# Performance work log

Measured on AMD Instinct MI355X. Metric: run time of the kernel, lower is better.

The kernel has to match this reference:

```python
import jax, jax.numpy as jnp
import numpy as np

B, N, E, L, H, FA = 64, 29, 812, 9, 256, 5  # batch, max atoms, edges, layers, hidden, atom types
SCALE = 15.0


def _scatter_add(vals, idx):
    # vals [B,E,D], idx [B,E] -> [B,N,D]  (replaces one-hot multiply + reduce_sum)
    return jax.vmap(lambda v, i: jnp.zeros((N, v.shape[-1]), v.dtype).at[i].add(v))(vals, idx)


def _align(x, mask):
    n = jnp.sum(mask, axis=1, keepdims=True)
    mean = jnp.sum(x, axis=1, keepdims=True) / n
    return (x - mean) * mask


def setup_inputs() -> dict:
    key = jax.random.key(0)
    ks = iter(jax.random.split(key, 32))
    # fully connected edges i != j, same graph per batch element
    pairs = np.array([(i, j) for i in range(N) for j in range(N) if i != j], dtype=np.int32)
    edge_indices = jnp.tile(jnp.asarray(pairs)[None], (B, 1, 1))
    x_in = jax.random.normal(next(ks), (B, N, 3), jnp.float32)
    h_in = jax.random.normal(next(ks), (B, N, FA), jnp.float32)
    t = jax.random.uniform(next(ks), (B, N, 1), jnp.float32)
    node_mask = jnp.ones((B, N, 1), jnp.float32)
    edge_mask = jnp.ones((B, E, 1), jnp.float32)

    def w(k, shape, fan):
        return jax.random.normal(k, shape, jnp.float32) / np.float32(np.sqrt(fan))

    params = dict(
        win_w=w(next(ks), (FA + 1, H), FA + 1), win_b=jnp.zeros((H,), jnp.float32),
        wout_w=w(next(ks), (H, FA + 1), H), wout_b=jnp.zeros((FA + 1,), jnp.float32),
        e_w1=w(next(ks), (L, 2 * H + 2, H), 2 * H + 2), e_b1=jnp.zeros((L, H), jnp.float32),
        e_w2=w(next(ks), (L, H, H), H), e_b2=jnp.zeros((L, H), jnp.float32),
        att_w=w(next(ks), (L, H, 1), H), att_b=jnp.zeros((L, 1), jnp.float32),
        h_w1=w(next(ks), (L, 2 * H, H), 2 * H), h_b1=jnp.zeros((L, H), jnp.float32),
        h_w2=w(next(ks), (L, H, H), H), h_b2=jnp.zeros((L, H), jnp.float32),
        x_w1=w(next(ks), (L, 2 * H + 2, H), 2 * H + 2), x_b1=jnp.zeros((L, H), jnp.float32),
        x_w2=w(next(ks), (L, H, H), H), x_b2=jnp.zeros((L, H), jnp.float32),
        x_w3=w(next(ks), (L, H, 1), H),
    )
    return {"x_in": x_in, "h_in": h_in, "t": t, "node_mask": node_mask,
            "edge_mask": edge_mask, "edge_indices": edge_indices, **params}


def _forward(x_in, h_in, t, node_mask, edge_mask, edge_indices, p):
    bidx = jnp.arange(x_in.shape[0])[:, None]
    idx_i, idx_j = edge_indices[..., 0], edge_indices[..., 1]
    h = jnp.concatenate([h_in, t], axis=-1) @ p["win_w"] + p["win_b"]
    x = x_in
    # global pairwise distances, masked (the `a` feature)
    xi0, xj0 = x[bidx, idx_i], x[bidx, idx_j]
    a = jnp.sqrt(jnp.sum((xi0 - xj0) ** 2, axis=-1, keepdims=True)) * edge_mask
    for l in range(L):
        x_i, x_j = x[bidx, idx_i], x[bidx, idx_j]
        diff = (x_i - x_j) * edge_mask              # [B,E,3]
        d = jnp.sqrt(jnp.sum(diff ** 2, axis=-1, keepdims=True))
        h_i, h_j = h[bidx, idx_i], h[bidx, idx_j]
        feat = jnp.concatenate([h_i, h_j, d ** 2, a], axis=-1)  # [B,E,514]
        # --- update_x ---
        u = jax.nn.silu(feat @ p["x_w1"][l] + p["x_b1"][l])
        u = jax.nn.silu(u @ p["x_w2"][l] + p["x_b2"][l])
        u = jnp.tanh(u @ p["x_w3"][l]) * SCALE      # [B,E,1]
        u = u * diff / (d + 1.0)                    # [B,E,3]
        x = (x + _scatter_add(u, idx_i)) * node_mask
        # --- update_h ---
        m = jax.nn.silu(feat @ p["e_w1"][l] + p["e_b1"][l])
        m = jax.nn.silu(m @ p["e_w2"][l] + p["e_b2"][l])
        e = jax.nn.sigmoid(m @ p["att_w"][l] + p["att_b"][l])
        agg = _scatter_add(e * m, idx_i)            # [B,N,256]
        hm = jax.nn.silu(jnp.concatenate([h, agg], axis=-1) @ p["h_w1"][l] + p["h_b1"][l])
        hm = hm @ p["h_w2"][l] + p["h_b2"][l]
        h = (h + hm) * node_mask
    x_out = _align((x - x_in) * node_mask, node_mask)
    h_out = (h @ p["wout_w"] + p["wout_b"]) * node_mask
    return jnp.concatenate([x_out, h_out[..., :-1]], axis=-1)


def reference(x_in, h_in, t, node_mask, edge_mask, edge_indices,
              win_w, win_b, wout_w, wout_b,
              e_w1, e_b1, e_w2, e_b2, att_w, att_b,
              h_w1, h_b1, h_w2, h_b2,
              x_w1, x_b1, x_w2, x_b2, x_w3):
    p = dict(win_w=win_w, win_b=win_b, wout_w=wout_w, wout_b=wout_b,
             e_w1=e_w1, e_b1=e_b1, e_w2=e_w2, e_b2=e_b2,
             att_w=att_w, att_b=att_b,
             h_w1=h_w1, h_b1=h_b1, h_w2=h_w2, h_b2=h_b2,
             x_w1=x_w1, x_b1=x_b1, x_w2=x_w2, x_b2=x_b2, x_w3=x_w3)
    return _forward(x_in, h_in, t, node_mask, edge_mask, edge_indices, p)
```

## Files before the change

kernel.cpp:

```cpp
#include <hip/hip_runtime.h>
#include <math.h>

#define B_ 64
#define N_ 29
#define E_ 812
#define L_ 9
#define H_ 256
#define FA_ 5
#define BN_ (B_*N_)
#define BE_ (B_*E_)
#define DEG_ 28
#define NBAND_ (BN_/64)
#define SCALE_ 15.0f

typedef __attribute__((ext_vector_type(8))) short bf16x8;
typedef __attribute__((ext_vector_type(4))) float f32x4;

__device__ __forceinline__ float sigmoidf_(float v){ return 1.0f/(1.0f+expf(-v)); }
__device__ __forceinline__ float siluf_(float v){ return v/(1.0f+expf(-v)); }
__device__ __forceinline__ float fsilu_(float v){
    float e = __expf(-v);
    return v * __builtin_amdgcn_rcpf(1.0f + e);
}

__device__ __forceinline__ ushort f2bf(float f){
    uint u = __float_as_uint(f);
    u += 0x7fffu + ((u>>16)&1u);
    return (ushort)(u>>16);
}
__device__ __forceinline__ float bf2f(ushort h){ return __uint_as_float(((uint)h)<<16); }

__global__ void k_init_h(const float* __restrict__ h_in, const float* __restrict__ t,
                         const float* __restrict__ win_w, const float* __restrict__ win_b,
                         float* __restrict__ h)
{
    int node = blockIdx.x; int c = threadIdx.x;
    float in[6];
    #pragma unroll
    for (int k=0;k<FA_;k++) in[k] = h_in[node*FA_+k];
    in[5] = t[node];
    float acc = win_b[c];
    #pragma unroll
    for (int k=0;k<6;k++) acc += in[k]*win_w[k*H_+c];
    h[(size_t)node*H_+c] = acc;
}

__global__ void k_init_xa(const float* __restrict__ x_in, const int* __restrict__ eidx,
                          const float* __restrict__ emask, float* __restrict__ x, float* __restrict__ a)
{
    int gid = blockIdx.x*256 + threadIdx.x;
    if (gid < BN_*3) x[gid] = x_in[gid];
    if (gid < BE_) {
        int b = gid / E_;
        int ii = eidx[2*gid], jj = eidx[2*gid+1];
        const float* xi = x_in + (size_t)(b*N_+ii)*3;
        const float* xj = x_in + (size_t)(b*N_+jj)*3;
        float dx = xi[0]-xj[0], dy = xi[1]-xj[1], dz = xi[2]-xj[2];
        a[gid] = sqrtf(dx*dx+dy*dy+dz*dz) * emask[gid];
    }
}

__global__ void k_wprep(const float* __restrict__ xw2, const float* __restrict__ ew2,
                        ushort* __restrict__ WfU, ushort* __restrict__ WfM)
{
    int gid = blockIdx.x*256 + threadIdx.x;
    if (gid >= L_*2*8192) return;
    int lane = gid & 63;
    int rest = gid >> 6;
    int ct = rest & 15; rest >>= 4;
    int ks = rest & 7;  rest >>= 3;
    int p  = rest & 1;  int l = rest >> 1;
    const float* src = (p ? ew2 : xw2) + (size_t)l*H_*H_;
    ushort* dst = (p ? WfM : WfU) + (size_t)l*131072;
    int g = lane>>4, li = lane&15;
    int col = ct*16 + li;
    int kb  = ks*32 + g*8;
    size_t fo = ((size_t)(ks*16+ct)*64 + lane)*8;
    ushort* dh = dst + fo;
    ushort* dl = dst + 65536 + fo;
    #pragma unroll
    for (int j=0;j<8;j++){
        float v = src[(size_t)(kb+j)*H_ + col];
        ushort h = f2bf(v);
        dh[j] = h;
        dl[j] = f2bf(v - bf2f(h));
    }
}

__global__ void k_wprep6(const float* __restrict__ xw1, const float* __restrict__ ew1,
                         const float* __restrict__ hw1, ushort* __restrict__ Wf6)
{
    int gid = blockIdx.x*256 + threadIdx.x;
    if (gid >= L_*5*8192) return;
    int lane = gid & 63;
    int rest = gid >> 6;
    int ct = rest & 15; rest >>= 4;
    int ks = rest & 7;  rest >>= 3;
    int m  = rest % 5;  int l = rest / 5;
    const float* src;
    switch (m) {
        case 0: src = xw1 + (size_t)l*514*H_; break;
        case 1: src = xw1 + (size_t)l*514*H_ + (size_t)256*H_; break;
        case 2: src = ew1 + (size_t)l*514*H_; break;
        case 3: src = ew1 + (size_t)l*514*H_ + (size_t)256*H_; break;
        default: src = hw1 + (size_t)l*512*H_; break;
    }
    ushort* dst = Wf6 + (size_t)(l*5+m)*196608;
    int g = lane>>4, li = lane&15;
    int col = ct*16 + li;
    int kb  = ks*32 + g*8;
    size_t fo = ((size_t)(ks*16+ct)*64 + lane)*8;
    #pragma unroll
    for (int j=0;j<8;j++){
        float v = src[(size_t)(kb+j)*H_ + col];
        ushort h0 = f2bf(v); float r1 = v - bf2f(h0);
        ushort h1 = f2bf(r1); float r2 = r1 - bf2f(h1);
        dst[fo+j] = h0;
        dst[65536+fo+j] = h1;
        dst[131072+fo+j] = f2bf(r2);
    }
}

__global__ void k_hfrag(const float* __restrict__ h,
                        ushort* __restrict__ p0, ushort* __restrict__ p1, ushort* __restrict__ p2)
{
    int gid = blockIdx.x*256 + threadIdx.x;
    if (gid >= BN_*32) return;
    int row = gid >> 5, octet = gid & 31;
    const float* src = h + (size_t)row*H_ + octet*8;
    int band=row>>6, r=row&63, rt=r>>4, li=r&15;
    int ks=octet>>2, gg=octet&3;
    size_t fo = (((size_t)((band*8+ks)*4+rt)*64)+(gg*16+li))*8;
    ushort q0[8], q1[8], q2[8];
    #pragma unroll
    for (int j=0;j<8;j++){
        float v = src[j];
        ushort h0 = f2bf(v); float r1 = v - bf2f(h0);
        ushort h1 = f2bf(r1); float r2 = r1 - bf2f(h1);
        q0[j]=h0; q1[j]=h1; q2[j]=f2bf(r2);
    }
    *(ushort4*)(p0+fo)   = make_ushort4(q0[0],q0[1],q0[2],q0[3]);
    *(ushort4*)(p0+fo+4) = make_ushort4(q0[4],q0[5],q0[6],q0[7]);
    *(ushort4*)(p1+fo)   = make_ushort4(q1[0],q1[1],q1[2],q1[3]);
    *(ushort4*)(p1+fo+4) = make_ushort4(q1[4],q1[5],q1[6],q1[7]);
    *(ushort4*)(p2+fo)   = make_ushort4(q2[0],q2[1],q2[2],q2[3]);
    *(ushort4*)(p2+fo+4) = make_ushort4(q2[4],q2[5],q2[6],q2[7]);
}

struct GArg { const float* A; const float* Bw; const float* bias; const float* add; const float* rmask; float* C; };
struct GArgs { GArg g[6]; };

template<int ACT>
__global__ __launch_bounds__(256)
void k_gemm64(GArgs args, int M, int Kdim)
{
    const GArg ga = args.g[blockIdx.z];
    __shared__ float As[16*68];
    __shared__ float Bs[16*68];
    const int tid = threadIdx.x;
    const int row0 = blockIdx.x*64;
    const int col0 = blockIdx.y*64;
    const int ty = tid>>4, tx = tid&15;
    const int am = tid>>2, ak = (tid&3)<<2;
    const int bk = tid>>4, bn = (tid&15)<<2;
    float acc[4][4] = {};
    const float* Ap = ga.A + (size_t)min(row0+am, M-1)*Kdim + ak;
    const float* Bp = ga.Bw + (size_t)bk*H_ + col0 + bn;
    for (int k0=0; k0<Kdim; k0+=16) {
        float4 av = *(const float4*)(Ap + k0);
        float4 bv = *(const float4*)(Bp + (size_t)k0*H_);
        __syncthreads();
        As[(ak+0)*68+am]=av.x; As[(ak+1)*68+am]=av.y; As[(ak+2)*68+am]=av.z; As[(ak+3)*68+am]=av.w;
        *(float4*)&Bs[bk*68+bn] = bv;
        __syncthreads();
        #pragma unroll
        for (int k=0;k<16;k++) {
            float4 a4 = *(const float4*)&As[k*68 + (ty<<2)];
            float4 b4 = *(const float4*)&Bs[k*68 + (tx<<2)];
            float aa[4]={a4.x,a4.y,a4.z,a4.w};
            float bb[4]={b4.x,b4.y,b4.z,b4.w};
            #pragma unroll
            for (int i=0;i<4;i++)
                #pragma unroll
                for (int j=0;j<4;j++)
                    acc[i][j] = fmaf(aa[i], bb[j], acc[i][j]);
        }
    }
    const int r0 = row0 + (ty<<2);
    const int c0 = col0 + (tx<<2);
    float4 bias4 = make_float4(0.f,0.f,0.f,0.f);
    if (ga.bias) bias4 = *(const float4*)(ga.bias + c0);
    #pragma unroll
    for (int i=0;i<4;i++) {
        int r = r0+i;
        if (r >= M) break;
        float v0=acc[i][0]+bias4.x, v1=acc[i][1]+bias4.y, v2=acc[i][2]+bias4.z, v3=acc[i][3]+bias4.w;
        if (ga.add) {
            float4 ad = *(const float4*)(ga.add + (size_t)r*H_ + c0);
            v0+=ad.x; v1+=ad.y; v2+=ad.z; v3+=ad.w;
        }
        if (ACT==1) { v0=siluf_(v0); v1=siluf_(v1); v2=siluf_(v2); v3=siluf_(v3); }
        if (ga.rmask) { float mv = ga.rmask[r]; v0*=mv; v1*=mv; v2*=mv; v3*=mv; }
        *(float4*)(ga.C + (size_t)r*H_ + c0) = make_float4(v0,v1,v2,v3);
    }
}

struct NArg6 { const ushort* A0; const ushort* A1; const ushort* A2;
               const ushort* Wf; float* Cf; };
struct NArgs6 { NArg6 g[5]; };

__global__ __launch_bounds__(256, 4)
void k_ngemm6(NArgs6 args)
{
    const NArg6 ga = args.g[blockIdx.z];
    const int tid  = threadIdx.x;
    const int lane = tid & 63;
    const int wv   = tid >> 6;
    const int g    = lane >> 4;
    const int li   = lane & 15;
    const int band = blockIdx.x;
    const int row0 = band*64;
    const int ctg  = blockIdx.y*4 + wv;

    const size_t abase = (size_t)band*16384 + (size_t)lane*8;
    const ushort* bp = ga.Wf + (size_t)ctg*512 + (size_t)lane*8;

    f32x4 acc[4];
    #pragma unroll
    for (int rt=0;rt<4;++rt) acc[rt] = (f32x4){0.f,0.f,0.f,0.f};

    #pragma unroll
    for (int ks=0; ks<8; ++ks){
        bf16x8 a0[4], a1[4], a2[4];
        #pragma unroll
        for (int rt=0; rt<4; ++rt){
            size_t o = abase + (size_t)(ks*4+rt)*512;
            a0[rt] = *(const bf16x8*)(ga.A0 + o);
            a1[rt] = *(const bf16x8*)(ga.A1 + o);
            a2[rt] = *(const bf16x8*)(ga.A2 + o);
        }
        bf16x8 b0 = *(const bf16x8*)(bp + ks*8192);
        bf16x8 b1 = *(const bf16x8*)(bp + 65536 + ks*8192);
        bf16x8 b2 = *(const bf16x8*)(bp + 131072 + ks*8192);
        #pragma unroll
        for (int rt=0; rt<4; ++rt){
            acc[rt] = __builtin_amdgcn_mfma_f32_16x16x32_bf16(a0[rt], b0, acc[rt], 0,0,0);
            acc[rt] = __builtin_amdgcn_mfma_f32_16x16x32_bf16(a1[rt], b0, acc[rt], 0,0,0);
            acc[rt] = __builtin_amdgcn_mfma_f32_16x16x32_bf16(a0[rt], b1, acc[rt], 0,0,0);
            acc[rt] = __builtin_amdgcn_mfma_f32_16x16x32_bf16(a1[rt], b1, acc[rt], 0,0,0);
            acc[rt] = __builtin_amdgcn_mfma_f32_16x16x32_bf16(a2[rt], b0, acc[rt], 0,0,0);
            acc[rt] = __builtin_amdgcn_mfma_f32_16x16x32_bf16(a0[rt], b2, acc[rt], 0,0,0);
        }
    }

    const int col = ctg*16 + li;
    #pragma unroll
    for (int rt=0; rt<4; ++rt){
        #pragma unroll
        for (int rg=0; rg<4; ++rg){
            int row = row0 + rt*16 + g*4 + rg;
            ga.Cf[(size_t)row*H_ + col] = acc[rt][rg];
        }
    }
}

__device__ __forceinline__ void frag_compute(
    const float* __restrict__ Xi, const float* __restrict__ Xj,
    const float* __restrict__ w5p, const float* __restrict__ w6p, const float* __restrict__ bp,
    int ni, int nj, float d2, float av, bool valid,
    int rt, int ks0, int lane,
    ushort (*fragH)[2][64][8], ushort (*fragL)[2][64][8])
{
    const int g = lane >> 4;
    if (valid){
        const float* xi = Xi + (size_t)ni*H_;
        const float* xj = Xj + (size_t)nj*H_;
        #pragma unroll
        for (int kq=0; kq<4; ++kq){
            int ks = ks0 + kq;
            int kb = ks*32 + g*8;
            float4 i0 = *(const float4*)(xi + kb),  i1 = *(const float4*)(xi + kb + 4);
            float4 j0 = *(const float4*)(xj + kb),  j1 = *(const float4*)(xj + kb + 4);
            float4 w50= *(const float4*)(w5p + kb), w51= *(const float4*)(w5p + kb + 4);
            float4 w60= *(const float4*)(w6p + kb), w61= *(const float4*)(w6p + kb + 4);
            float4 b0 = *(const float4*)(bp + kb),  b1v= *(const float4*)(bp + kb + 4);
            float v[8];
            v[0]=fsilu_(i0.x+j0.x+d2*w50.x+av*w60.x+b0.x);
            v[1]=fsilu_(i0.y+j0.y+d2*w50.y+av*w60.y+b0.y);
            v[2]=fsilu_(i0.z+j0.z+d2*w50.z+av*w60.z+b0.z);
            v[3]=fsilu_(i0.w+j0.w+d2*w50.w+av*w60.w+b0.w);
            v[4]=fsilu_(i1.x+j1.x+d2*w51.x+av*w61.x+b1v.x);
            v[5]=fsilu_(i1.y+j1.y+d2*w51.y+av*w61.y+b1v.y);
            v[6]=fsilu_(i1.z+j1.z+d2*w51.z+av*w61.z+b1v.z);
            v[7]=fsilu_(i1.w+j1.w+d2*w51.w+av*w61.w+b1v.w);
            ushort hh[8], ll[8];
            #pragma unroll
            for (int q=0;q<8;q++){ hh[q]=f2bf(v[q]); ll[q]=f2bf(v[q]-bf2f(hh[q])); }
            *(ushort4*)&fragH[ks][rt][lane][0] = make_ushort4(hh[0],hh[1],hh[2],hh[3]);
            *(ushort4*)&fragH[ks][rt][lane][4] = make_ushort4(hh[4],hh[5],hh[6],hh[7]);
            *(ushort4*)&fragL[ks][rt][lane][0] = make_ushort4(ll[0],ll[1],ll[2],ll[3]);
            *(ushort4*)&fragL[ks][rt][lane][4] = make_ushort4(ll[4],ll[5],ll[6],ll[7]);
        }
    } else {
        ushort4 z4 = make_ushort4(0,0,0,0);
        #pragma unroll
        for (int kq=0; kq<4; ++kq){
            int ks = ks0 + kq;
            *(ushort4*)&fragH[ks][rt][lane][0] = z4;
            *(ushort4*)&fragH[ks][rt][lane][4] = z4;
            *(ushort4*)&fragL[ks][rt][lane][0] = z4;
            *(ushort4*)&fragL[ks][rt][lane][4] = z4;
        }
    }
}

__device__ __forceinline__ void mfma_lds(
    const ushort (*fragH)[2][64][8], const ushort (*fragL)[2][64][8],
    const ushort* __restrict__ bp, int lane, f32x4 (&acc)[2][4])
{
    bf16x8 bh[2][4], bl[2][4];
    #pragma unroll
    for (int ct=0; ct<4; ++ct){
        bh[0][ct] = *(const bf16x8*)(bp + ct*512);
        bl[0][ct] = *(const bf16x8*)(bp + 65536 + ct*512);
    }
    #pragma unroll
    for (int ks=0; ks<8; ++ks){
        const int cur = ks & 1;
        const int nxt = cur ^ 1;
        if (ks < 7){
            #pragma unroll
            for (int ct=0; ct<4; ++ct){
                bh[nxt][ct] = *(const bf16x8*)(bp + (ks+1)*8192 + ct*512);
                bl[nxt][ct] = *(const bf16x8*)(bp + 65536 + (ks+1)*8192 + ct*512);
            }
        }
        bf16x8 ah[2], al[2];
        #pragma unroll
        for (int rt=0; rt<2; ++rt){
            ah[rt] = *(const bf16x8*)&fragH[ks][rt][lane][0];
            al[rt] = *(const bf16x8*)&fragL[ks][rt][lane][0];
        }
        #pragma unroll
        for (int ct=0; ct<4; ++ct){
            #pragma unroll
            for (int rt=0; rt<2; ++rt){
                acc[rt][ct] = __builtin_amdgcn_mfma_f32_16x16x32_bf16(ah[rt], bh[cur][ct], acc[rt][ct], 0,0,0);
                acc[rt][ct] = __builtin_amdgcn_mfma_f32_16x16x32_bf16(al[rt], bh[cur][ct], acc[rt][ct], 0,0,0);
                acc[rt][ct] = __builtin_amdgcn_mfma_f32_16x16x32_bf16(ah[rt], bl[cur][ct], acc[rt][ct], 0,0,0);
            }
        }
    }
}

__global__ __launch_bounds__(256, 4)
void k_edge_mega(const float* __restrict__ XHi, const float* __restrict__ XHj,
                 const float* __restrict__ EHi, const float* __restrict__ EHj,
                 const float* __restrict__ x_cur, const float* __restrict__ a,
                 const int* __restrict__ eidx, const float* __restrict__ emask,
                 const float* __restrict__ nmask,
                 const float* __restrict__ xw512, const float* __restrict__ xw513, const float* __restrict__ xb1,
                 const float* __restrict__ ew512, const float* __restrict__ ew513, const float* __restrict__ eb1,
                 const ushort* __restrict__ WfU, const ushort* __restrict__ WfM,
                 const float* __restrict__ xb2, const float* __restrict__ xw3,
                 const float* __restrict__ eb2, const float* __restrict__ attw,
                 const float* __restrict__ attb,
                 float* __restrict__ x_new, float* __restrict__ agg)
{
    __shared__ __align__(16) ushort fragH[8][2][64][8];
    __shared__ __align__(16) ushort fragL[8][2][64][8];
    __shared__ float pdLds[2][4][32];
    __shared__ float easLds[32];
    __shared__ float cxyz[DEG_][3];

    const int tid  = threadIdx.x;
    const int lane = tid & 63;
    const int wv   = tid >> 6;
    const int g    = lane >> 4;
    const int li   = lane & 15;
    const int rt   = wv & 1;
    const int ks0  = (wv >> 1)*4;
    const int n0   = blockIdx.x;

    const int frow = rt*16 + li;
    const bool valid = (frow < DEG_);
    int nj=0; float d2=0.f, av=0.f;
    if (valid){
        int bb = n0 / N_;
        size_t ge = (size_t)n0*DEG_ + frow;
        int jj = eidx[2*ge+1];
        nj = bb*N_ + jj;
        float em = emask[ge];
        float dx=(x_cur[n0*3+0]-x_cur[nj*3+0])*em;
        float dy=(x_cur[n0*3+1]-x_cur[nj*3+1])*em;
        float dz=(x_cur[n0*3+2]-x_cur[nj*3+2])*em;
        d2 = dx*dx+dy*dy+dz*dz;
        av = a[ge];
    }

    const ushort* bpU = WfU + ((size_t)(wv*4)*64 + lane)*8;
    const ushort* bpM = WfM + ((size_t)(wv*4)*64 + lane)*8;

    f32x4 acc[2][4];

    frag_compute(XHi, XHj, xw512, xw513, xb1, n0, nj, d2, av, valid, rt, ks0, lane, fragH, fragL);
    __syncthreads();

    #pragma unroll
    for (int r=0;r<2;++r)
        #pragma unroll
        for (int ct=0;ct<4;++ct)
            acc[r][ct] = (f32x4){0.f,0.f,0.f,0.f};
    mfma_lds(fragH, fragL, bpU, lane, acc);
    {
        float pdv[2][4];
        #pragma unroll
        for (int r=0;r<2;++r)
            #pragma unroll
            for (int rg=0;rg<4;++rg) pdv[r][rg]=0.f;
        #pragma unroll
        for (int ct=0; ct<4; ++ct){
            const int col = wv*64 + ct*16 + li;
            const float bi = xb2[col];
            const float wvv = xw3[col];
            #pragma unroll
            for (int r=0; r<2; ++r)
                #pragma unroll
                for (int rg=0; rg<4; ++rg)
                    pdv[r][rg] += fsilu_(acc[r][ct][rg] + bi)*wvv;
        }
        #pragma unroll
        for (int r=0;r<2;++r)
            #pragma unroll
            for (int rg=0;rg<4;++rg){
                float s = pdv[r][rg];
                s += __shfl_xor(s, 1, 16);
                s += __shfl_xor(s, 2, 16);
                s += __shfl_xor(s, 4, 16);
                s += __shfl_xor(s, 8, 16);
                if (li==0) pdLds[0][wv][r*16 + g*4 + rg] = s;
            }
    }
    __syncthreads();

    frag_compute(EHi, EHj, ew512, ew513, eb1, n0, nj, d2, av, valid, rt, ks0, lane, fragH, fragL);
    __syncthreads();

    #pragma unroll
    for (int r=0;r<2;++r)
        #pragma unroll
        for (int ct=0;ct<4;++ct)
            acc[r][ct] = (f32x4){0.f,0.f,0.f,0.f};
    mfma_lds(fragH, fragL, bpM, lane, acc);
    {
        float pdv[2][4];
        #pragma unroll
        for (int r=0;r<2;++r)
            #pragma unroll
            for (int rg=0;rg<4;++rg) pdv[r][rg]=0.f;
        #pragma unroll
        for (int ct=0; ct<4; ++ct){
            const int col = wv*64 + ct*16 + li;
            const float bi = eb2[col];
            const float wvv = attw[col];
            #pragma unroll
            for (int r=0; r<2; ++r)
                #pragma unroll
                for (int rg=0; rg<4; ++rg){
                    float v = fsilu_(acc[r][ct][rg] + bi);
                    acc[r][ct][rg] = v;
                    pdv[r][rg] += v*wvv;
                }
        }
        #pragma unroll
        for (int r=0;r<2;++r)
            #pragma unroll
            for (int rg=0;rg<4;++rg){
                float s = pdv[r][rg];
                s += __shfl_xor(s, 1, 16);
                s += __shfl_xor(s, 2, 16);
                s += __shfl_xor(s, 4, 16);
                s += __shfl_xor(s, 8, 16);
                if (li==0) pdLds[1][wv][r*16 + g*4 + rg] = s;
            }
    }
    __syncthreads();

    if (wv == 0){
        int t = lane;
        if (t < 32){
            float ea = 0.f;
            if (t < DEG_){
                float sU = pdLds[0][0][t]+pdLds[0][1][t]+pdLds[0][2][t]+pdLds[0][3][t];
                float sM = pdLds[1][0][t]+pdLds[1][1][t]+pdLds[1][2][t]+pdLds[1][3][t];
                float tsc = tanhf(sU)*SCALE_;
                ea = sigmoidf_(sM + attb[0]);
                size_t ge = (size_t)n0*DEG_ + t;
                int bb = n0 / N_;
                int jj = eidx[2*ge+1];
                int njs = bb*N_ + jj;
                float em = emask[ge];
                float dx=(x_cur[n0*3+0]-x_cur[njs*3+0])*em;
                float dy=(x_cur[n0*3+1]-x_cur[njs*3+1])*em;
                float dz=(x_cur[n0*3+2]-x_cur[njs*3+2])*em;
                float dd = sqrtf(dx*dx+dy*dy+dz*dz);
                float sc = tsc/(dd+1.0f);
                cxyz[t][0]=sc*dx; cxyz[t][1]=sc*dy; cxyz[t][2]=sc*dz;
            }
            easLds[t] = ea;
        }
        if (t == 0){
            float sx=0.f, sy=0.f, sz=0.f;
            #pragma unroll 4
            for (int k=0;k<DEG_;k++){ sx+=cxyz[k][0]; sy+=cxyz[k][1]; sz+=cxyz[k][2]; }
            float nm = nmask[n0];
            x_new[n0*3+0]=(x_cur[n0*3+0]+sx)*nm;
            x_new[n0*3+1]=(x_cur[n0*3+1]+sy)*nm;
            x_new[n0*3+2]=(x_cur[n0*3+2]+sz)*nm;
        }
    }
    __syncthreads();

    float p[4] = {0.f,0.f,0.f,0.f};
    #pragma unroll
    for (int r=0; r<2; ++r){
        #pragma unroll
        for (int rg=0; rg<4; ++rg){
            int row = r*16 + g*4 + rg;
            float w = easLds[row];
            #pragma unroll
            for (int ct=0; ct<4; ++ct)
                p[ct] += w*acc[r][ct][rg];
        }
    }
    #pragma unroll
    for (int ct=0; ct<4; ++ct){
        p[ct] += __shfl_xor(p[ct], 16);
        p[ct] += __shfl_xor(p[ct], 32);
    }
    if (g == 0){
        #pragma unroll
        for (int ct=0; ct<4; ++ct){
            int col = wv*64 + ct*16 + li;
            agg[(size_t)n0*H_ + col] = p[ct];
        }
    }
}

__global__ void k_out_x(const float* __restrict__ x, const float* __restrict__ x_in,
                        const float* __restrict__ nmask, float* __restrict__ out)
{
    int b = blockIdx.x; int l = threadIdx.x;
    int row = b*N_ + l;
    float xd0=0.f,xd1=0.f,xd2=0.f,nm=0.f;
    if (l < N_) {
        nm = nmask[row];
        xd0 = (x[(size_t)row*3+0]-x_in[(size_t)row*3+0])*nm;
        xd1 = (x[(size_t)row*3+1]-x_in[(size_t)row*3+1])*nm;
        xd2 = (x[(size_t)row*3+2]-x_in[(size_t)row*3+2])*nm;
    }
    float s0=xd0,s1=xd1,s2=xd2,sn=nm;
    #pragma unroll
    for (int off=32; off; off>>=1) {
        s0+=__shfl_xor(s0,off,64); s1+=__shfl_xor(s1,off,64);
        s2+=__shfl_xor(s2,off,64); sn+=__shfl_xor(sn,off,64);
    }
    float m0=s0/sn, m1=s1/sn, m2=s2/sn;
    if (l < N_) {
        out[(size_t)row*8+0]=(xd0-m0)*nm;
        out[(size_t)row*8+1]=(xd1-m1)*nm;
        out[(size_t)row*8+2]=(xd2-m2)*nm;
    }
}

__global__ void k_out_h(const float* __restrict__ h, const float* __restrict__ wout_w, const float* __restrict__ wout_b,
                        const float* __restrict__ nmask, float* __restrict__ out)
{
    int row = blockIdx.x; int lane = threadIdx.x;
    int c4 = lane<<2;
    float4 hv = *(const float4*)(h + (size_t)row*H_ + c4);
    float p0=0,p1=0,p2=0,p3=0,p4=0;
    float hvv[4] = {hv.x,hv.y,hv.z,hv.w};
    #pragma unroll
    for (int j=0;j<4;j++) {
        int k = c4+j;
        float hval = hvv[j];
        p0 += hval * wout_w[k*6+0];
        p1 += hval * wout_w[k*6+1];
        p2 += hval * wout_w[k*6+2];
        p3 += hval * wout_w[k*6+3];
        p4 += hval * wout_w[k*6+4];
    }
    #pragma unroll
    for (int off=32; off; off>>=1) {
        p0+=__shfl_xor(p0,off,64); p1+=__shfl_xor(p1,off,64); p2+=__shfl_xor(p2,off,64);
        p3+=__shfl_xor(p3,off,64); p4+=__shfl_xor(p4,off,64);
    }
    if (lane==0) {
        float nm = nmask[row];
        out[(size_t)row*8+3] = (p0+wout_b[0])*nm;
        out[(size_t)row*8+4] = (p1+wout_b[1])*nm;
        out[(size_t)row*8+5] = (p2+wout_b[2])*nm;
        out[(size_t)row*8+6] = (p3+wout_b[3])*nm;
        out[(size_t)row*8+7] = (p4+wout_b[4])*nm;
    }
}

extern "C" void kernel_launch(void* const* d_in, const int* in_sizes, int n_in,
                              void* d_out, int out_size, void* d_ws, size_t ws_size,
                              hipStream_t stream)
{
    const float* x_in  = (const float*)d_in[0];
    const float* h_in  = (const float*)d_in[1];
    const float* t     = (const float*)d_in[2];
    const float* nmask = (const float*)d_in[3];
    const float* emask = (const float*)d_in[4];
    const int*   eidx  = (const int*)d_in[5];
    const float* win_w = (const float*)d_in[6];
    const float* win_b = (const float*)d_in[7];
    const float* wout_w= (const float*)d_in[8];
    const float* wout_b= (const float*)d_in[9];
    const float* e_w1  = (const float*)d_in[10];
    const float* e_b1  = (const float*)d_in[11];
    const float* e_w2  = (const float*)d_in[12];
    const float* e_b2  = (const float*)d_in[13];
    const float* att_w = (const float*)d_in[14];
    const float* att_b = (const float*)d_in[15];
    const float* h_w1  = (const float*)d_in[16];
    const float* h_b1  = (const float*)d_in[17];
    const float* h_w2  = (const float*)d_in[18];
    const float* h_b2  = (const float*)d_in[19];
    const float* x_w1  = (const float*)d_in[20];
    const float* x_b1  = (const float*)d_in[21];
    const float* x_w2  = (const float*)d_in[22];
    const float* x_b2  = (const float*)d_in[23];
    const float* x_w3  = (const float*)d_in[24];
    float* out = (float*)d_out;

    char* ws = (char*)d_ws;
    size_t off = 0;
    auto alloc = [&](size_t bytes)->float* {
        float* p = (float*)(ws + off);
        off = (off + bytes + 255) & ~(size_t)255;
        return p;
    };
    const size_t PLANE = (size_t)NBAND_*16384;
    float*  h     = alloc((size_t)BN_*H_*4);
    ushort* hp0   = (ushort*)alloc(PLANE*2);
    ushort* hp1   = (ushort*)alloc(PLANE*2);
    ushort* hp2   = (ushort*)alloc(PLANE*2);
    float*  xA    = alloc((size_t)BN_*3*4);
    float*  xB    = alloc((size_t)BN_*3*4);
    float*  a     = alloc((size_t)BE_*4);
    float*  NB5   = alloc((size_t)5*BN_*H_*4);
    float*  agg   = alloc((size_t)BN_*H_*4);
    float*  hm1   = alloc((size_t)BN_*H_*4);
    ushort* WfU   = (ushort*)alloc((size_t)L_*131072*sizeof(ushort));
    ushort* WfM   = (ushort*)alloc((size_t)L_*131072*sizeof(ushort));
    ushort* Wf6   = (ushort*)alloc((size_t)L_*5*196608*sizeof(ushort));

    k_init_h<<<BN_, H_, 0, stream>>>(h_in, t, win_w, win_b, h);
    k_init_xa<<<(BE_+255)/256, 256, 0, stream>>>(x_in, eidx, emask, xA, a);
    k_wprep<<<(L_*2*8192+255)/256, 256, 0, stream>>>(x_w2, e_w2, WfU, WfM);
    k_wprep6<<<(L_*5*8192+255)/256, 256, 0, stream>>>(x_w1, e_w1, h_w1, Wf6);

    float* x_cur = xA;
    float* x_new = xB;

    for (int l=0; l<L_; l++) {
        const float* xw1l = x_w1 + (size_t)l*514*H_;
        const float* ew1l = e_w1 + (size_t)l*514*H_;
        const float* hw1l = h_w1 + (size_t)l*512*H_;
        const ushort* Wl6 = Wf6 + (size_t)l*5*196608;

        float* XHi=NB5;
        float* XHj=NB5+(size_t)BN_*H_;
        float* EHi=NB5+(size_t)2*BN_*H_;
        float* EHj=NB5+(size_t)3*BN_*H_;
        float* Htop=NB5+(size_t)4*BN_*H_;

        k_hfrag<<<(BN_*32+255)/256, 256, 0, stream>>>(h, hp0, hp1, hp2);

        NArgs6 na = {};
        for (int z=0; z<5; z++){
            na.g[z].A0=hp0; na.g[z].A1=hp1; na.g[z].A2=hp2;
            na.g[z].Wf = Wl6 + (size_t)z*196608;
            na.g[z].Cf = NB5 + (size_t)z*BN_*H_;
        }
        k_ngemm6<<<dim3(NBAND_,4,5),256,0,stream>>>(na);

        k_edge_mega<<<BN_, 256, 0, stream>>>(XHi, XHj, EHi, EHj, x_cur, a,
            eidx, emask, nmask,
            xw1l+(size_t)512*H_, xw1l+(size_t)513*H_, x_b1+(size_t)l*H_,
            ew1l+(size_t)512*H_, ew1l+(size_t)513*H_, e_b1+(size_t)l*H_,
            WfU + (size_t)l*131072, WfM + (size_t)l*131072,
            x_b2+(size_t)l*H_, x_w3+(size_t)l*H_,
            e_b2+(size_t)l*H_, att_w+(size_t)l*H_, att_b+l,
            x_new, agg);

        GArgs ha = {};
        ha.g[0] = { agg, hw1l+(size_t)256*H_, h_b1+(size_t)l*H_, Htop, nullptr, hm1 };
        k_gemm64<1><<<dim3(BN_/64,H_/64,1),256,0,stream>>>(ha, BN_, H_);

        GArgs h2 = {};
        h2.g[0] = { hm1, h_w2+(size_t)l*H_*H_, h_b2+(size_t)l*H_, h, nmask, h };
        k_gemm64<0><<<dim3(BN_/64,H_/64,1),256,0,stream>>>(h2, BN_, H_);

        float* tmp = x_cur; x_cur = x_new; x_new = tmp;
    }

    k_out_x<<<B_,64,0,stream>>>(x_cur, x_in, nmask, out);
    k_out_h<<<BN_,64,0,stream>>>(h, wout_w, wout_b, nmask, out);
}
```

Before: 1.155 ms.

## Split edge-MLP K loop into halves to halve LDS and raise occupancy

The edge megakernel now computes the bf16 hi/lo activation fragments and runs the MFMA accumulation in two K-halves, so the fragH/fragL LDS buffers shrink to half size. The double-buffered B-fragment prefetch registers are dropped, and launch bounds go from 4 to 8 blocks per SM. The aim is higher occupancy, with more resident blocks to hide latency. The cost is two extra block-wide barriers per GEMM, no software prefetch of weights, and possible register spilling under the tighter launch bound.

```diff
diff --git a/kernel.cpp b/kernel.cpp
--- a/kernel.cpp
+++ b/kernel.cpp
@@ -264,11 +264,11 @@
     }
 }
 
-__device__ __forceinline__ void frag_compute(
+__device__ __forceinline__ void frag_half(
     const float* __restrict__ Xi, const float* __restrict__ Xj,
     const float* __restrict__ w5p, const float* __restrict__ w6p, const float* __restrict__ bp,
     int ni, int nj, float d2, float av, bool valid,
-    int rt, int ks0, int lane,
+    int rt, int ksl0, int khalf, int lane,
     ushort (*fragH)[2][64][8], ushort (*fragL)[2][64][8])
 {
     const int g = lane >> 4;
@@ -276,9 +276,10 @@
         const float* xi = Xi + (size_t)ni*H_;
         const float* xj = Xj + (size_t)nj*H_;
         #pragma unroll
-        for (int kq=0; kq<4; ++kq){
-            int ks = ks0 + kq;
-            int kb = ks*32 + g*8;
+        for (int kq=0; kq<2; ++kq){
+            int ksl = ksl0 + kq;
+            int ks  = khalf*4 + ksl;
+            int kb  = ks*32 + g*8;
             float4 i0 = *(const float4*)(xi + kb),  i1 = *(const float4*)(xi + kb + 4);
             float4 j0 = *(const float4*)(xj + kb),  j1 = *(const float4*)(xj + kb + 4);
             float4 w50= *(const float4*)(w5p + kb), w51= *(const float4*)(w5p + kb + 4);
@@ -296,64 +297,52 @@
             ushort hh[8], ll[8];
             #pragma unroll
             for (int q=0;q<8;q++){ hh[q]=f2bf(v[q]); ll[q]=f2bf(v[q]-bf2f(hh[q])); }
-            *(ushort4*)&fragH[ks][rt][lane][0] = make_ushort4(hh[0],hh[1],hh[2],hh[3]);
-            *(ushort4*)&fragH[ks][rt][lane][4] = make_ushort4(hh[4],hh[5],hh[6],hh[7]);
-            *(ushort4*)&fragL[ks][rt][lane][0] = make_ushort4(ll[0],ll[1],ll[2],ll[3]);
-            *(ushort4*)&fragL[ks][rt][lane][4] = make_ushort4(ll[4],ll[5],ll[6],ll[7]);
+            *(ushort4*)&fragH[ksl][rt][lane][0] = make_ushort4(hh[0],hh[1],hh[2],hh[3]);
+            *(ushort4*)&fragH[ksl][rt][lane][4] = make_ushort4(hh[4],hh[5],hh[6],hh[7]);
+            *(ushort4*)&fragL[ksl][rt][lane][0] = make_ushort4(ll[0],ll[1],ll[2],ll[3]);
+            *(ushort4*)&fragL[ksl][rt][lane][4] = make_ushort4(ll[4],ll[5],ll[6],ll[7]);
         }
     } else {
         ushort4 z4 = make_ushort4(0,0,0,0);
         #pragma unroll
-        for (int kq=0; kq<4; ++kq){
-            int ks = ks0 + kq;
-            *(ushort4*)&fragH[ks][rt][lane][0] = z4;
-            *(ushort4*)&fragH[ks][rt][lane][4] = z4;
-            *(ushort4*)&fragL[ks][rt][lane][0] = z4;
-            *(ushort4*)&fragL[ks][rt][lane][4] = z4;
-        }
-    }
-}
-
-__device__ __forceinline__ void mfma_lds(
+        for (int kq=0; kq<2; ++kq){
+            int ksl = ksl0 + kq;
+            *(ushort4*)&fragH[ksl][rt][lane][0] = z4;
+            *(ushort4*)&fragH[ksl][rt][lane][4] = z4;
+            *(ushort4*)&fragL[ksl][rt][lane][0] = z4;
+            *(ushort4*)&fragL[ksl][rt][lane][4] = z4;
+        }
+    }
+}
+
+__device__ __forceinline__ void mfma_half(
     const ushort (*fragH)[2][64][8], const ushort (*fragL)[2][64][8],
-    const ushort* __restrict__ bp, int lane, f32x4 (&acc)[2][4])
-{
-    bf16x8 bh[2][4], bl[2][4];
-    #pragma unroll
-    for (int ct=0; ct<4; ++ct){
-        bh[0][ct] = *(const bf16x8*)(bp + ct*512);
-        bl[0][ct] = *(const bf16x8*)(bp + 65536 + ct*512);
-    }
-    #pragma unroll
-    for (int ks=0; ks<8; ++ks){
-        const int cur = ks & 1;
-        const int nxt = cur ^ 1;
-        if (ks < 7){
-            #pragma unroll
-            for (int ct=0; ct<4; ++ct){
-                bh[nxt][ct] = *(const bf16x8*)(bp + (ks+1)*8192 + ct*512);
-                bl[nxt][ct] = *(const bf16x8*)(bp + 65536 + (ks+1)*8192 + ct*512);
+    const ushort* __restrict__ bp, int khalf, int lane, f32x4 (&acc)[2][4])
+{
+    #pragma unroll
+    for (int ksl=0; ksl<4; ++ksl){
+        const int ks = khalf*4 + ksl;
+        bf16x8 ah[2], al[2];
+        #pragma unroll
+        for (int rt=0; rt<2; ++rt){
+            ah[rt] = *(const bf16x8*)&fragH[ksl][rt][lane][0];
+            al[rt] = *(const bf16x8*)&fragL[ksl][rt][lane][0];
+        }
+        #pragma unroll
+        for (int ct=0; ct<4; ++ct){
+            bf16x8 bh = *(const bf16x8*)(bp + ks*8192 + ct*512);
+            bf16x8 bl = *(const bf16x8*)(bp + 65536 + ks*8192 + ct*512);
+            #pragma unroll
+            for (int rt=0; rt<2; ++rt){
+                acc[rt][ct] = __builtin_amdgcn_mfma_f32_16x16x32_bf16(ah[rt], bh, acc[rt][ct], 0,0,0);
+                acc[rt][ct] = __builtin_amdgcn_mfma_f32_16x16x32_bf16(al[rt], bh, acc[rt][ct], 0,0,0);
+                acc[rt][ct] = __builtin_amdgcn_mfma_f32_16x16x32_bf16(ah[rt], bl, acc[rt][ct], 0,0,0);
             }
         }
-        bf16x8 ah[2], al[2];
-        #pragma unroll
-        for (int rt=0; rt<2; ++rt){
-            ah[rt] = *(const bf16x8*)&fragH[ks][rt][lane][0];
-            al[rt] = *(const bf16x8*)&fragL[ks][rt][lane][0];
-        }
-        #pragma unroll
-        for (int ct=0; ct<4; ++ct){
-            #pragma unroll
-            for (int rt=0; rt<2; ++rt){
-                acc[rt][ct] = __builtin_amdgcn_mfma_f32_16x16x32_bf16(ah[rt], bh[cur][ct], acc[rt][ct], 0,0,0);
-                acc[rt][ct] = __builtin_amdgcn_mfma_f32_16x16x32_bf16(al[rt], bh[cur][ct], acc[rt][ct], 0,0,0);
-                acc[rt][ct] = __builtin_amdgcn_mfma_f32_16x16x32_bf16(ah[rt], bl[cur][ct], acc[rt][ct], 0,0,0);
-            }
-        }
-    }
-}
-
-__global__ __launch_bounds__(256, 4)
+    }
+}
+
+__global__ __launch_bounds__(256, 8)
 void k_edge_mega(const float* __restrict__ XHi, const float* __restrict__ XHj,
                  const float* __restrict__ EHi, const float* __restrict__ EHj,
                  const float* __restrict__ x_cur, const float* __restrict__ a,
@@ -367,8 +356,8 @@
                  const float* __restrict__ attb,
                  float* __restrict__ x_new, float* __restrict__ agg)
 {
-    __shared__ __align__(16) ushort fragH[8][2][64][8];
-    __shared__ __align__(16) ushort fragL[8][2][64][8];
+    __shared__ __align__(16) ushort fragH[4][2][64][8];
+    __shared__ __align__(16) ushort fragL[4][2][64][8];
     __shared__ float pdLds[2][4][32];
     __shared__ float easLds[32];
     __shared__ float cxyz[DEG_][3];
@@ -379,7 +368,7 @@
     const int g    = lane >> 4;
     const int li   = lane & 15;
     const int rt   = wv & 1;
-    const int ks0  = (wv >> 1)*4;
+    const int ksl0 = (wv >> 1)*2;
     const int n0   = blockIdx.x;
 
     const int frow = rt*16 + li;
@@ -403,15 +392,18 @@
 
     f32x4 acc[2][4];
 
-    frag_compute(XHi, XHj, xw512, xw513, xb1, n0, nj, d2, av, valid, rt, ks0, lane, fragH, fragL);
-    __syncthreads();
-
     #pragma unroll
     for (int r=0;r<2;++r)
         #pragma unroll
         for (int ct=0;ct<4;++ct)
             acc[r][ct] = (f32x4){0.f,0.f,0.f,0.f};
-    mfma_lds(fragH, fragL, bpU, lane, acc);
+    #pragma unroll
+    for (int kh=0; kh<2; ++kh){
+        frag_half(XHi, XHj, xw512, xw513, xb1, n0, nj, d2, av, valid, rt, ksl0, kh, lane, fragH, fragL);
+        __syncthreads();
+        mfma_half(fragH, fragL, bpU, kh, lane, acc);
+        __syncthreads();
+    }
     {
         float pdv[2][4];
         #pragma unroll
@@ -443,15 +435,18 @@
     }
     __syncthreads();
 
-    frag_compute(EHi, EHj, ew512, ew513, eb1, n0, nj, d2, av, valid, rt, ks0, lane, fragH, fragL);
-    __syncthreads();
-
     #pragma unroll
     for (int r=0;r<2;++r)
         #pragma unroll
         for (int ct=0;ct<4;++ct)
             acc[r][ct] = (f32x4){0.f,0.f,0.f,0.f};
-    mfma_lds(fragH, fragL, bpM, lane, acc);
+    #pragma unroll
+    for (int kh=0; kh<2; ++kh){
+        frag_half(EHi, EHj, ew512, ew513, eb1, n0, nj, d2, av, valid, rt, ksl0, kh, lane, fragH, fragL);
+        __syncthreads();
+        mfma_half(fragH, fragL, bpM, kh, lane, acc);
+        __syncthreads();
+    }
     {
         float pdv[2][4];
         #pragma unroll
```

Result: slower. 1.705 ms (+47.6%).
